# Kernel optimization log

Hardware: AMD Instinct MI355X
Metric: run time of the kernel (lower is better)

Reference implementation:

```python
import jax, jax.numpy as jnp
import numpy as np

B, T, D, H = 2, 2048, 1024, 16  # batch, seq, n_embed, n_head


def setup_inputs() -> dict:
    key = jax.random.key(0)
    ks = jax.random.split(key, 5)
    scale = 1.0 / np.sqrt(D)
    return {
        "x": jax.random.normal(ks[0], (B, T, D), dtype=jnp.float32),
        "Wq": jax.random.normal(ks[1], (D, D), dtype=jnp.float32) * scale,
        "Wk": jax.random.normal(ks[2], (D, D), dtype=jnp.float32) * scale,
        "Wv": jax.random.normal(ks[3], (D, D), dtype=jnp.float32) * scale,
        "Wo": jax.random.normal(ks[4], (D, D), dtype=jnp.float32) * scale,
    }


def reference(x, Wq, Wk, Wv, Wo):
    b, t, d = x.shape
    hd = d // H  # head_dim
    # projections -> [B, H, T, hd]
    q = (x @ Wq).reshape(b, t, H, hd).transpose(0, 2, 1, 3)
    k = (x @ Wk).reshape(b, t, H, hd).transpose(0, 2, 1, 3)
    v = (x @ Wv).reshape(b, t, H, hd).transpose(0, 2, 1, 3)
    # scaled scores [B, H, T, T] with causal mask
    e = jnp.einsum("bhqd,bhkd->bhqk", q, k) * (1.0 / np.sqrt(hd))
    causal = jnp.tril(jnp.ones((t, t), dtype=bool))
    e = jnp.where(causal[None, None], e, jnp.finfo(e.dtype).min)
    alpha = jax.nn.softmax(e, axis=-1)
    # attention output -> [B, T, D]
    attn = jnp.einsum("bhqk,bhkd->bhqd", alpha, v)
    attn = attn.transpose(0, 2, 1, 3).reshape(b, t, d)
    return attn @ Wo
```

## Files before the change

kernel.cpp:

```cpp
#include <hip/hip_runtime.h>
#include <hip/hip_bf16.h>
#include <math.h>


#define Bsz  2
#define Tseq 2048
#define Dm   1024
#define NH   16
#define HD   64

typedef short bf16x8 __attribute__((ext_vector_type(8)));
typedef float floatx4 __attribute__((ext_vector_type(4)));

__device__ __forceinline__ unsigned short f2bf(float f) {
    __hip_bfloat16 h = __float2bfloat16(f);
    return *reinterpret_cast<unsigned short*>(&h);
}

__device__ __forceinline__ unsigned short f2bf_fast(float f) {
    unsigned int u = __builtin_bit_cast(unsigned int, f);
    return (unsigned short)((u + 0x8000u) >> 16);
}

__device__ __forceinline__ void lds16(unsigned short* lds, const unsigned short* g) {
    __builtin_amdgcn_global_load_lds(
        (const __attribute__((address_space(1))) void*)g,
        (__attribute__((address_space(3))) void*)lds, 16, 0, 0);
}

__global__ __launch_bounds__(256) void prep(const float* __restrict__ x,
                                            const float* __restrict__ W0,
                                            const float* __restrict__ W1,
                                            const float* __restrict__ W2,
                                            const float* __restrict__ W3,
                                            unsigned short* __restrict__ xb,
                                            unsigned short* __restrict__ T0,
                                            unsigned short* __restrict__ T1,
                                            unsigned short* __restrict__ T2,
                                            unsigned short* __restrict__ T3) {
    __shared__ float t[64][65];
    const int z = blockIdx.z;
    if (z >= 4) {
        const int bi = (z - 4) * 256 + blockIdx.y * 16 + blockIdx.x;
        const size_t i = (size_t)bi * 256 + threadIdx.x;
        const float4 v = ((const float4*)x)[i];
        ushort4 o;
        o.x = f2bf(v.x); o.y = f2bf(v.y); o.z = f2bf(v.z); o.w = f2bf(v.w);
        ((ushort4*)xb)[i] = o;
        return;
    }
    const float* W = (z == 0) ? W0 : (z == 1) ? W1 : (z == 2) ? W2 : W3;
    unsigned short* T = (z == 0) ? T0 : (z == 1) ? T1 : (z == 2) ? T2 : T3;
    const int k0 = blockIdx.y * 64, n0 = blockIdx.x * 64;
    const int row = threadIdx.x >> 6, col = threadIdx.x & 63;
#pragma unroll
    for (int p = 0; p < 16; ++p)
        t[p * 4 + row][col] = W[(size_t)(k0 + p * 4 + row) * Dm + n0 + col];
    __syncthreads();
#pragma unroll
    for (int p = 0; p < 16; ++p)
        T[(size_t)(n0 + p * 4 + row) * Dm + k0 + col] = f2bf(t[col][p * 4 + row]);
}

__device__ __forceinline__ void gemm128_mainloop(const unsigned short* __restrict__ A,
                                                 const unsigned short* __restrict__ Bt,
                                                 int K, int m0, int n0,
                                                 unsigned short* As, unsigned short* Bs,
                                                 floatx4 acc[4][4]) {
    const int tid = threadIdx.x;
    const int lane = tid & 63, wave = tid >> 6;
    const int l15 = lane & 15, quad = lane >> 4;
    const int wm = (wave >> 1) * 64, wn = (wave & 1) * 64;

    for (int k0 = 0; k0 < K; k0 += 32) {
        __syncthreads();
#pragma unroll
        for (int c = 0; c < 2; ++c) {
            const int idx = c * 256 + tid;
            const int row = idx >> 2, kc = (idx & 3) * 8;
            lds16(&As[row * 32 + kc], A + (size_t)(m0 + row) * K + k0 + kc);
            lds16(&Bs[row * 32 + kc], Bt + (size_t)(n0 + row) * K + k0 + kc);
        }
        __syncthreads();
        bf16x8 af[4], bf[4];
#pragma unroll
        for (int i = 0; i < 4; ++i)
            af[i] = *(const bf16x8*)&As[(wm + i * 16 + l15) * 32 + quad * 8];
#pragma unroll
        for (int j = 0; j < 4; ++j)
            bf[j] = *(const bf16x8*)&Bs[(wn + j * 16 + l15) * 32 + quad * 8];
#pragma unroll
        for (int i = 0; i < 4; ++i)
#pragma unroll
            for (int j = 0; j < 4; ++j)
                acc[i][j] = __builtin_amdgcn_mfma_f32_16x16x32_bf16(af[i], bf[j], acc[i][j], 0, 0, 0);
    }
}

__global__ __launch_bounds__(256) void gemm_qkv(const unsigned short* __restrict__ xb,
                                                const unsigned short* __restrict__ Wqt,
                                                const unsigned short* __restrict__ Wkt,
                                                const unsigned short* __restrict__ Wvt,
                                                unsigned short* __restrict__ Qb,
                                                unsigned short* __restrict__ Kb,
                                                unsigned short* __restrict__ VbT) {
    __shared__ unsigned short As[128 * 32];
    __shared__ unsigned short Bs[128 * 32];
    const int z = blockIdx.z;
    const unsigned short* Bt = (z == 0) ? Wqt : (z == 1) ? Wkt : Wvt;
    const float scale = (z == 0) ? (0.125f * 1.4426950408889634f) : 1.0f;
    const int m0 = blockIdx.y * 128, n0 = blockIdx.x * 128;

    floatx4 acc[4][4];
#pragma unroll
    for (int i = 0; i < 4; ++i)
#pragma unroll
        for (int j = 0; j < 4; ++j) acc[i][j] = (floatx4){0.f, 0.f, 0.f, 0.f};

    gemm128_mainloop(xb, Bt, Dm, m0, n0, As, Bs, acc);

    const int lane = threadIdx.x & 63, wave = threadIdx.x >> 6;
    const int l15 = lane & 15, quad = lane >> 4;
    const int wm = (wave >> 1) * 64, wn = (wave & 1) * 64;

    if (z == 2) {
#pragma unroll
        for (int i = 0; i < 4; ++i)
#pragma unroll
            for (int j = 0; j < 4; ++j) {
                const int col = n0 + wn + j * 16 + l15;
                const int hh = col >> 6, dd = col & 63;
                const int tok = m0 + wm + i * 16 + quad * 4;
                const int bb = tok >> 11, tl = tok & (Tseq - 1);
                ushort4 o;
                o.x = f2bf(acc[i][j][0]); o.y = f2bf(acc[i][j][1]);
                o.z = f2bf(acc[i][j][2]); o.w = f2bf(acc[i][j][3]);
                *(ushort4*)&VbT[((size_t)((bb * NH + hh) * HD + dd)) * Tseq + tl] = o;
            }
        return;
    }
    unsigned short* C = (z == 0) ? Qb : Kb;
#pragma unroll
    for (int i = 0; i < 4; ++i)
#pragma unroll
        for (int j = 0; j < 4; ++j)
#pragma unroll
            for (int r = 0; r < 4; ++r) {
                const int row = m0 + wm + i * 16 + quad * 4 + r;
                const int col = n0 + wn + j * 16 + l15;
                C[(size_t)row * Dm + col] = f2bf(acc[i][j][r] * scale);
            }
}

__global__ __launch_bounds__(256) void gemm_out(const unsigned short* __restrict__ Yb,
                                                const unsigned short* __restrict__ Wot,
                                                float* __restrict__ out) {
    __shared__ unsigned short As[128 * 32];
    __shared__ unsigned short Bs[64 * 32];
    const int m0 = blockIdx.y * 128, n0 = blockIdx.x * 64;
    const int tid = threadIdx.x;
    const int lane = tid & 63, wave = tid >> 6;
    const int l15 = lane & 15, quad = lane >> 4;
    const int wm = (wave >> 1) * 64, wn = (wave & 1) * 32;

    floatx4 acc[4][2];
#pragma unroll
    for (int i = 0; i < 4; ++i)
#pragma unroll
        for (int j = 0; j < 2; ++j) acc[i][j] = (floatx4){0.f, 0.f, 0.f, 0.f};

    for (int k0 = 0; k0 < Dm; k0 += 32) {
        __syncthreads();
        {
#pragma unroll
            for (int c = 0; c < 2; ++c) {
                const int idx = c * 256 + tid;
                const int row = idx >> 2, kc = (idx & 3) * 8;
                lds16(&As[row * 32 + kc], Yb + (size_t)(m0 + row) * Dm + k0 + kc);
            }
            const int row = tid >> 2, kc = (tid & 3) * 8;
            lds16(&Bs[row * 32 + kc], Wot + (size_t)(n0 + row) * Dm + k0 + kc);
        }
        __syncthreads();
        bf16x8 af[4], bf[2];
#pragma unroll
        for (int i = 0; i < 4; ++i)
            af[i] = *(const bf16x8*)&As[(wm + i * 16 + l15) * 32 + quad * 8];
#pragma unroll
        for (int j = 0; j < 2; ++j)
            bf[j] = *(const bf16x8*)&Bs[(wn + j * 16 + l15) * 32 + quad * 8];
#pragma unroll
        for (int i = 0; i < 4; ++i)
#pragma unroll
            for (int j = 0; j < 2; ++j)
                acc[i][j] = __builtin_amdgcn_mfma_f32_16x16x32_bf16(af[i], bf[j], acc[i][j], 0, 0, 0);
    }

#pragma unroll
    for (int i = 0; i < 4; ++i)
#pragma unroll
        for (int j = 0; j < 2; ++j)
#pragma unroll
            for (int r = 0; r < 4; ++r) {
                const int row = m0 + wm + i * 16 + quad * 4 + r;
                const int col = n0 + wn + j * 16 + l15;
                out[(size_t)row * Dm + col] = acc[i][j][r];
            }
}

__global__ __launch_bounds__(256) void attn_mfma(const unsigned short* __restrict__ Qb,
                                                 const unsigned short* __restrict__ Kb,
                                                 const unsigned short* __restrict__ VbT,
                                                 unsigned short* __restrict__ Yb) {
    const int bh = blockIdx.x;
    const int b = bh >> 4;
    const int h = bh & 15;
    const int qt = 31 - blockIdx.y;
    const int tid = threadIdx.x;
    const int wave = tid >> 6;
    const int lane = tid & 63;
    const int l15 = lane & 15;
    const int quad = lane >> 4;

    __shared__ unsigned short Ks0[64][32];
    __shared__ unsigned short Ks1[64][32];
    __shared__ unsigned short Vt0[64][32];
    __shared__ unsigned short Vt1[64][32];
    __shared__ unsigned short Ps[4][16][72];

    const size_t tok0 = (size_t)b * Tseq;
    const int colh = h * HD;
    const unsigned short* vbase = VbT + (size_t)bh * HD * Tseq;

    const int qrow = qt * 64 + wave * 16;

    const unsigned short* qptr = Qb + (tok0 + qrow + l15) * Dm + colh + quad * 8;
    const bf16x8 qf0 = *(const bf16x8*)(qptr);
    const bf16x8 qf1 = *(const bf16x8*)(qptr + 32);

    float l_lane[4] = {0.f, 0.f, 0.f, 0.f};
    floatx4 o_acc[4];
#pragma unroll
    for (int t = 0; t < 4; ++t) o_acc[t] = (floatx4){0.f, 0.f, 0.f, 0.f};

    const int srow = tid >> 2;
    const int sc8 = (tid & 3) * 8;

    for (int kt = 0; kt <= qt; ++kt) {
        const int k0 = kt * 64;
        __syncthreads();
        {
            const unsigned short* krow = Kb + (tok0 + k0 + srow) * Dm + colh;
            const unsigned short* vrow = vbase + (size_t)srow * Tseq + k0;
            lds16(&Ks0[srow][sc8], krow + sc8);
            lds16(&Ks1[srow][sc8], krow + 32 + sc8);
            lds16(&Vt0[srow][sc8], vrow + sc8);
            lds16(&Vt1[srow][sc8], vrow + 32 + sc8);
        }
        __syncthreads();

        floatx4 s[4];
#pragma unroll
        for (int t = 0; t < 4; ++t) {
            floatx4 c = (floatx4){0.f, 0.f, 0.f, 0.f};
            const bf16x8 b0 = *(const bf16x8*)&Ks0[t * 16 + l15][quad * 8];
            const bf16x8 b1 = *(const bf16x8*)&Ks1[t * 16 + l15][quad * 8];
            c = __builtin_amdgcn_mfma_f32_16x16x32_bf16(qf0, b0, c, 0, 0, 0);
            c = __builtin_amdgcn_mfma_f32_16x16x32_bf16(qf1, b1, c, 0, 0, 0);
            s[t] = c;
        }

        if (kt == qt) {
#pragma unroll
            for (int t = 0; t < 4; ++t)
#pragma unroll
                for (int r = 0; r < 4; ++r) {
                    const int kl = t * 16 + l15;
                    const int ql = wave * 16 + quad * 4 + r;
                    if (kl > ql) s[t][r] = -1.0e30f;
                }
        }

#pragma unroll
        for (int t = 0; t < 4; ++t)
#pragma unroll
            for (int r = 0; r < 4; ++r) {
                const float p = __builtin_amdgcn_exp2f(s[t][r]);
                l_lane[r] += p;
                Ps[wave][quad * 4 + r][t * 16 + l15] = f2bf_fast(p);
            }

        const bf16x8 pa0 = *(const bf16x8*)&Ps[wave][l15][quad * 8];
        const bf16x8 pa1 = *(const bf16x8*)&Ps[wave][l15][32 + quad * 8];
#pragma unroll
        for (int t = 0; t < 4; ++t) {
            const bf16x8 vb0 = *(const bf16x8*)&Vt0[t * 16 + l15][quad * 8];
            const bf16x8 vb1 = *(const bf16x8*)&Vt1[t * 16 + l15][quad * 8];
            o_acc[t] = __builtin_amdgcn_mfma_f32_16x16x32_bf16(pa0, vb0, o_acc[t], 0, 0, 0);
            o_acc[t] = __builtin_amdgcn_mfma_f32_16x16x32_bf16(pa1, vb1, o_acc[t], 0, 0, 0);
        }
    }

#pragma unroll
    for (int off = 1; off < 16; off <<= 1)
#pragma unroll
        for (int r = 0; r < 4; ++r)
            l_lane[r] += __shfl_xor(l_lane[r], off);
    float inv_l[4];
#pragma unroll
    for (int r = 0; r < 4; ++r) inv_l[r] = 1.0f / l_lane[r];
#pragma unroll
    for (int t = 0; t < 4; ++t)
#pragma unroll
        for (int r = 0; r < 4; ++r) {
            const int q = qrow + quad * 4 + r;
            Yb[(tok0 + q) * Dm + colh + t * 16 + l15] = f2bf(o_acc[t][r] * inv_l[r]);
        }
}

extern "C" void kernel_launch(void* const* d_in, const int* in_sizes, int n_in,
                              void* d_out, int out_size, void* d_ws, size_t ws_size,
                              hipStream_t stream) {
    const float* x  = (const float*)d_in[0];
    const float* Wq = (const float*)d_in[1];
    const float* Wk = (const float*)d_in[2];
    const float* Wv = (const float*)d_in[3];
    const float* Wo = (const float*)d_in[4];
    float* out = (float*)d_out;

    const int M = Bsz * Tseq;
    char* ws = (char*)d_ws;
    unsigned short* xb  = (unsigned short*)(ws);
    unsigned short* Wqt = (unsigned short*)(ws + (((size_t)8)  << 20));
    unsigned short* Wkt = (unsigned short*)(ws + (((size_t)10) << 20));
    unsigned short* Wvt = (unsigned short*)(ws + (((size_t)12) << 20));
    unsigned short* Wot = (unsigned short*)(ws + (((size_t)14) << 20));
    unsigned short* Qb  = (unsigned short*)(ws + (((size_t)16) << 20));
    unsigned short* Kb  = (unsigned short*)(ws + (((size_t)24) << 20));
    unsigned short* VbT = (unsigned short*)(ws + (((size_t)32) << 20));
    unsigned short* Yb  = (unsigned short*)(ws + (((size_t)40) << 20));

    dim3 blk(256);
    hipLaunchKernelGGL(prep, dim3(16, 16, 20), blk, 0, stream,
                       x, Wq, Wk, Wv, Wo, xb, Wqt, Wkt, Wvt, Wot);

    hipLaunchKernelGGL(gemm_qkv, dim3(Dm / 128, M / 128, 3), blk, 0, stream,
                       xb, Wqt, Wkt, Wvt, Qb, Kb, VbT);

    hipLaunchKernelGGL(attn_mfma, dim3(Bsz * NH, 32), blk, 0, stream, Qb, Kb, VbT, Yb);

    hipLaunchKernelGGL(gemm_out, dim3(Dm / 64, M / 128), blk, 0, stream, Yb, Wot, out);
}
```

Measured before the change: 177.2 us.

## Fuse QKV projections into one GEMM and process two key tiles per attention sync

```diff
diff --git a/kernel.cpp b/kernel.cpp
--- a/kernel.cpp
+++ b/kernel.cpp
@@ -62,41 +62,6 @@
         T[(size_t)(n0 + p * 4 + row) * Dm + k0 + col] = f2bf(t[col][p * 4 + row]);
 }
 
-__device__ __forceinline__ void gemm128_mainloop(const unsigned short* __restrict__ A,
-                                                 const unsigned short* __restrict__ Bt,
-                                                 int K, int m0, int n0,
-                                                 unsigned short* As, unsigned short* Bs,
-                                                 floatx4 acc[4][4]) {
-    const int tid = threadIdx.x;
-    const int lane = tid & 63, wave = tid >> 6;
-    const int l15 = lane & 15, quad = lane >> 4;
-    const int wm = (wave >> 1) * 64, wn = (wave & 1) * 64;
-
-    for (int k0 = 0; k0 < K; k0 += 32) {
-        __syncthreads();
-#pragma unroll
-        for (int c = 0; c < 2; ++c) {
-            const int idx = c * 256 + tid;
-            const int row = idx >> 2, kc = (idx & 3) * 8;
-            lds16(&As[row * 32 + kc], A + (size_t)(m0 + row) * K + k0 + kc);
-            lds16(&Bs[row * 32 + kc], Bt + (size_t)(n0 + row) * K + k0 + kc);
-        }
-        __syncthreads();
-        bf16x8 af[4], bf[4];
-#pragma unroll
-        for (int i = 0; i < 4; ++i)
-            af[i] = *(const bf16x8*)&As[(wm + i * 16 + l15) * 32 + quad * 8];
-#pragma unroll
-        for (int j = 0; j < 4; ++j)
-            bf[j] = *(const bf16x8*)&Bs[(wn + j * 16 + l15) * 32 + quad * 8];
-#pragma unroll
-        for (int i = 0; i < 4; ++i)
-#pragma unroll
-            for (int j = 0; j < 4; ++j)
-                acc[i][j] = __builtin_amdgcn_mfma_f32_16x16x32_bf16(af[i], bf[j], acc[i][j], 0, 0, 0);
-    }
-}
-
 __global__ __launch_bounds__(256) void gemm_qkv(const unsigned short* __restrict__ xb,
                                                 const unsigned short* __restrict__ Wqt,
                                                 const unsigned short* __restrict__ Wkt,
@@ -105,51 +70,85 @@
                                                 unsigned short* __restrict__ Kb,
                                                 unsigned short* __restrict__ VbT) {
     __shared__ unsigned short As[128 * 32];
-    __shared__ unsigned short Bs[128 * 32];
-    const int z = blockIdx.z;
-    const unsigned short* Bt = (z == 0) ? Wqt : (z == 1) ? Wkt : Wvt;
-    const float scale = (z == 0) ? (0.125f * 1.4426950408889634f) : 1.0f;
-    const int m0 = blockIdx.y * 128, n0 = blockIdx.x * 128;
-
-    floatx4 acc[4][4];
+    __shared__ unsigned short Bs[3][64 * 32];
+    const int m0 = blockIdx.y * 128, n0 = blockIdx.x * 64;
+    const int tid = threadIdx.x;
+    const int lane = tid & 63, wave = tid >> 6;
+    const int l15 = lane & 15, quad = lane >> 4;
+    const int wm = (wave >> 1) * 64, wn = (wave & 1) * 32;
+
+    const unsigned short* Wt[3] = {Wqt, Wkt, Wvt};
+
+    floatx4 acc[3][4][2];
+#pragma unroll
+    for (int zz = 0; zz < 3; ++zz)
+#pragma unroll
+        for (int i = 0; i < 4; ++i)
+#pragma unroll
+            for (int j = 0; j < 2; ++j) acc[zz][i][j] = (floatx4){0.f, 0.f, 0.f, 0.f};
+
+    const int arow0 = tid >> 2;
+    const int kc = (tid & 3) * 8;
+
+    for (int k0 = 0; k0 < Dm; k0 += 32) {
+        __syncthreads();
+#pragma unroll
+        for (int c = 0; c < 2; ++c) {
+            const int row = c * 64 + arow0;
+            lds16(&As[row * 32 + kc], xb + (size_t)(m0 + row) * Dm + k0 + kc);
+        }
+#pragma unroll
+        for (int zz = 0; zz < 3; ++zz)
+            lds16(&Bs[zz][arow0 * 32 + kc], Wt[zz] + (size_t)(n0 + arow0) * Dm + k0 + kc);
+        __syncthreads();
+
+        bf16x8 af[4];
+#pragma unroll
+        for (int i = 0; i < 4; ++i)
+            af[i] = *(const bf16x8*)&As[(wm + i * 16 + l15) * 32 + quad * 8];
+#pragma unroll
+        for (int zz = 0; zz < 3; ++zz) {
+            bf16x8 bf[2];
+#pragma unroll
+            for (int j = 0; j < 2; ++j)
+                bf[j] = *(const bf16x8*)&Bs[zz][(wn + j * 16 + l15) * 32 + quad * 8];
+#pragma unroll
+            for (int i = 0; i < 4; ++i)
+#pragma unroll
+                for (int j = 0; j < 2; ++j)
+                    acc[zz][i][j] = __builtin_amdgcn_mfma_f32_16x16x32_bf16(af[i], bf[j], acc[zz][i][j], 0, 0, 0);
+        }
+    }
+
+    const float qscale = 0.125f * 1.4426950408889634f;
+#pragma unroll
+    for (int zz = 0; zz < 2; ++zz) {
+        unsigned short* C = (zz == 0) ? Qb : Kb;
+        const float sc = (zz == 0) ? qscale : 1.0f;
+#pragma unroll
+        for (int i = 0; i < 4; ++i)
+#pragma unroll
+            for (int j = 0; j < 2; ++j)
+#pragma unroll
+                for (int r = 0; r < 4; ++r) {
+                    const int row = m0 + wm + i * 16 + quad * 4 + r;
+                    const int col = n0 + wn + j * 16 + l15;
+                    C[(size_t)row * Dm + col] = f2bf(acc[zz][i][j][r] * sc);
+                }
+    }
 #pragma unroll
     for (int i = 0; i < 4; ++i)
 #pragma unroll
-        for (int j = 0; j < 4; ++j) acc[i][j] = (floatx4){0.f, 0.f, 0.f, 0.f};
-
-    gemm128_mainloop(xb, Bt, Dm, m0, n0, As, Bs, acc);
-
-    const int lane = threadIdx.x & 63, wave = threadIdx.x >> 6;
-    const int l15 = lane & 15, quad = lane >> 4;
-    const int wm = (wave >> 1) * 64, wn = (wave & 1) * 64;
-
-    if (z == 2) {
-#pragma unroll
-        for (int i = 0; i < 4; ++i)
-#pragma unroll
-            for (int j = 0; j < 4; ++j) {
-                const int col = n0 + wn + j * 16 + l15;
-                const int hh = col >> 6, dd = col & 63;
-                const int tok = m0 + wm + i * 16 + quad * 4;
-                const int bb = tok >> 11, tl = tok & (Tseq - 1);
-                ushort4 o;
-                o.x = f2bf(acc[i][j][0]); o.y = f2bf(acc[i][j][1]);
-                o.z = f2bf(acc[i][j][2]); o.w = f2bf(acc[i][j][3]);
-                *(ushort4*)&VbT[((size_t)((bb * NH + hh) * HD + dd)) * Tseq + tl] = o;
-            }
-        return;
-    }
-    unsigned short* C = (z == 0) ? Qb : Kb;
-#pragma unroll
-    for (int i = 0; i < 4; ++i)
-#pragma unroll
-        for (int j = 0; j < 4; ++j)
-#pragma unroll
-            for (int r = 0; r < 4; ++r) {
-                const int row = m0 + wm + i * 16 + quad * 4 + r;
-                const int col = n0 + wn + j * 16 + l15;
-                C[(size_t)row * Dm + col] = f2bf(acc[i][j][r] * scale);
-            }
+        for (int j = 0; j < 2; ++j) {
+            const int col = n0 + wn + j * 16 + l15;
+            const int hh = col >> 6, dd = col & 63;
+            const int tok = m0 + wm + i * 16 + quad * 4;
+            const int bb = tok >> 11, tl = tok & (Tseq - 1);
+            ushort4 o;
+            o.x = f2bf(acc[2][i][j][0]); o.y = f2bf(acc[2][i][j][1]);
+            o.z = f2bf(acc[2][i][j][2]); o.w = f2bf(acc[2][i][j][3]);
+            *(ushort4*)&VbT[((size_t)((bb * NH + hh) * HD + dd)) * Tseq + tl] = o;
+        }
 }
 
 __global__ __launch_bounds__(256) void gemm_out(const unsigned short* __restrict__ Yb,
@@ -222,10 +221,10 @@
     const int l15 = lane & 15;
     const int quad = lane >> 4;
 
-    __shared__ unsigned short Ks0[64][32];
-    __shared__ unsigned short Ks1[64][32];
-    __shared__ unsigned short Vt0[64][32];
-    __shared__ unsigned short Vt1[64][32];
+    __shared__ unsigned short Ks0[2][64][32];
+    __shared__ unsigned short Ks1[2][64][32];
+    __shared__ unsigned short Vt0[2][64][32];
+    __shared__ unsigned short Vt1[2][64][32];
     __shared__ unsigned short Ps[4][16][72];
 
     const size_t tok0 = (size_t)b * Tseq;
@@ -246,58 +245,66 @@
     const int srow = tid >> 2;
     const int sc8 = (tid & 3) * 8;
 
-    for (int kt = 0; kt <= qt; ++kt) {
-        const int k0 = kt * 64;
-        __syncthreads();
-        {
-            const unsigned short* krow = Kb + (tok0 + k0 + srow) * Dm + colh;
-            const unsigned short* vrow = vbase + (size_t)srow * Tseq + k0;
-            lds16(&Ks0[srow][sc8], krow + sc8);
-            lds16(&Ks1[srow][sc8], krow + 32 + sc8);
-            lds16(&Vt0[srow][sc8], vrow + sc8);
-            lds16(&Vt1[srow][sc8], vrow + 32 + sc8);
-        }
-        __syncthreads();
-
-        floatx4 s[4];
-#pragma unroll
-        for (int t = 0; t < 4; ++t) {
-            floatx4 c = (floatx4){0.f, 0.f, 0.f, 0.f};
-            const bf16x8 b0 = *(const bf16x8*)&Ks0[t * 16 + l15][quad * 8];
-            const bf16x8 b1 = *(const bf16x8*)&Ks1[t * 16 + l15][quad * 8];
-            c = __builtin_amdgcn_mfma_f32_16x16x32_bf16(qf0, b0, c, 0, 0, 0);
-            c = __builtin_amdgcn_mfma_f32_16x16x32_bf16(qf1, b1, c, 0, 0, 0);
-            s[t] = c;
-        }
-
-        if (kt == qt) {
+    const int niter = (qt + 2) >> 1;
+    for (int it = 0; it < niter; ++it) {
+        const int k0 = it * 128;
+        __syncthreads();
+#pragma unroll
+        for (int s = 0; s < 2; ++s) {
+            const unsigned short* krow = Kb + (tok0 + k0 + s * 64 + srow) * Dm + colh;
+            const unsigned short* vrow = vbase + (size_t)srow * Tseq + k0 + s * 64;
+            lds16(&Ks0[s][srow][sc8], krow + sc8);
+            lds16(&Ks1[s][srow][sc8], krow + 32 + sc8);
+            lds16(&Vt0[s][srow][sc8], vrow + sc8);
+            lds16(&Vt1[s][srow][sc8], vrow + 32 + sc8);
+        }
+        __syncthreads();
+
+#pragma unroll
+        for (int s = 0; s < 2; ++s) {
+            const int k0s = k0 + s * 64;
+            if (k0s > qrow + 15) continue;
+
+            floatx4 sf[4];
+#pragma unroll
+            for (int t = 0; t < 4; ++t) {
+                floatx4 c = (floatx4){0.f, 0.f, 0.f, 0.f};
+                const bf16x8 b0 = *(const bf16x8*)&Ks0[s][t * 16 + l15][quad * 8];
+                const bf16x8 b1 = *(const bf16x8*)&Ks1[s][t * 16 + l15][quad * 8];
+                c = __builtin_amdgcn_mfma_f32_16x16x32_bf16(qf0, b0, c, 0, 0, 0);
+                c = __builtin_amdgcn_mfma_f32_16x16x32_bf16(qf1, b1, c, 0, 0, 0);
+                sf[t] = c;
+            }
+
+            if (k0s + 63 > qrow) {
+#pragma unroll
+                for (int t = 0; t < 4; ++t)
+#pragma unroll
+                    for (int r = 0; r < 4; ++r) {
+                        const int kl = k0s + t * 16 + l15;
+                        const int ql = qrow + quad * 4 + r;
+                        if (kl > ql) sf[t][r] = -1.0e30f;
+                    }
+            }
+
 #pragma unroll
             for (int t = 0; t < 4; ++t)
 #pragma unroll
                 for (int r = 0; r < 4; ++r) {
-                    const int kl = t * 16 + l15;
-                    const int ql = wave * 16 + quad * 4 + r;
-                    if (kl > ql) s[t][r] = -1.0e30f;
+                    const float p = __builtin_amdgcn_exp2f(sf[t][r]);
+                    l_lane[r] += p;
+                    Ps[wave][quad * 4 + r][t * 16 + l15] = f2bf_fast(p);
                 }
-        }
-
-#pragma unroll
-        for (int t = 0; t < 4; ++t)
-#pragma unroll
-            for (int r = 0; r < 4; ++r) {
-                const float p = __builtin_amdgcn_exp2f(s[t][r]);
-                l_lane[r] += p;
-                Ps[wave][quad * 4 + r][t * 16 + l15] = f2bf_fast(p);
-            }
-
-        const bf16x8 pa0 = *(const bf16x8*)&Ps[wave][l15][quad * 8];
-        const bf16x8 pa1 = *(const bf16x8*)&Ps[wave][l15][32 + quad * 8];
-#pragma unroll
-        for (int t = 0; t < 4; ++t) {
-            const bf16x8 vb0 = *(const bf16x8*)&Vt0[t * 16 + l15][quad * 8];
-            const bf16x8 vb1 = *(const bf16x8*)&Vt1[t * 16 + l15][quad * 8];
-            o_acc[t] = __builtin_amdgcn_mfma_f32_16x16x32_bf16(pa0, vb0, o_acc[t], 0, 0, 0);
-            o_acc[t] = __builtin_amdgcn_mfma_f32_16x16x32_bf16(pa1, vb1, o_acc[t], 0, 0, 0);
+
+            const bf16x8 pa0 = *(const bf16x8*)&Ps[wave][l15][quad * 8];
+            const bf16x8 pa1 = *(const bf16x8*)&Ps[wave][l15][32 + quad * 8];
+#pragma unroll
+            for (int t = 0; t < 4; ++t) {
+                const bf16x8 vb0 = *(const bf16x8*)&Vt0[s][t * 16 + l15][quad * 8];
+                const bf16x8 vb1 = *(const bf16x8*)&Vt1[s][t * 16 + l15][quad * 8];
+                o_acc[t] = __builtin_amdgcn_mfma_f32_16x16x32_bf16(pa0, vb0, o_acc[t], 0, 0, 0);
+                o_acc[t] = __builtin_amdgcn_mfma_f32_16x16x32_bf16(pa1, vb1, o_acc[t], 0, 0, 0);
+            }
         }
     }
 
@@ -344,7 +351,7 @@
     hipLaunchKernelGGL(prep, dim3(16, 16, 20), blk, 0, stream,
                        x, Wq, Wk, Wv, Wo, xb, Wqt, Wkt, Wvt, Wot);
 
-    hipLaunchKernelGGL(gemm_qkv, dim3(Dm / 128, M / 128, 3), blk, 0, stream,
+    hipLaunchKernelGGL(gemm_qkv, dim3(Dm / 64, M / 128), blk, 0, stream,
                        xb, Wqt, Wkt, Wvt, Qb, Kb, VbT);
 
     hipLaunchKernelGGL(attn_mfma, dim3(Bsz * NH, 32), blk, 0, stream, Qb, Kb, VbT, Yb);
```

Measured after the change: 201.4 us. +13.7%, slower.
